# Kernel optimization log

Measured on AMD Instinct MI355X. Metric: run time of the kernel, lower is better.

Reference implementation:

```python
import jax, jax.numpy as jnp
import numpy as np

NHEAD = 8
TOPKS = [16, 8]  # coarse -> fine (indexed by loop i over reversed pyramids)


def _gather_kv(t, idx):
    # t: [b, M, nh, d], idx: [b, N, K, nh] -> gathered [b, N, K, nh, d]
    b, M, nh, d = t.shape
    bi = jnp.arange(b)[:, None, None, None]
    hi = jnp.arange(nh)[None, None, None, :]
    return t[bi, idx, hi]


def _process_level(query, key, value, topk_pos, topk_prev, topk):
    # query: [b, c, h0, w0]; key/value: [b, c, h1, w1] with h1=h0, w1=w0
    bs, c, h0, w0 = query.shape
    _, _, h1, w1 = key.shape
    nh = NHEAD
    d = c // nh
    N = (h0 // 2) * (w0 // 2)
    # b c h w -> b (h w) nh d
    k = key.reshape(bs, c, h1 * w1).transpose(0, 2, 1).reshape(bs, h1 * w1, nh, d)
    v = value.reshape(bs, c, h1 * w1).transpose(0, 2, 1).reshape(bs, h1 * w1, nh, d)
    # b c (h 2) (w 2) -> b (h w) 4 nh d  (2x2 query groups)
    q = query.reshape(bs, c, h0 // 2, 2, w0 // 2, 2)
    q = q.transpose(0, 2, 4, 3, 5, 1).reshape(bs, N, 4, nh, d)
    # expand each coarse candidate position into its 2x2 children in the key grid
    tp = topk_pos * 2  # [2, b, N, Kp, nh]
    idx = jnp.stack([(tp[0] + x) * w1 + (tp[1] + y)
                     for x in (0, 1) for y in (0, 1)], axis=3)  # [b,N,Kp,4,nh]
    K = topk_prev * 4
    idx = idx.reshape(bs, N, K, nh)
    # sparse scores: QK[b,n,t,k,h] = <q[b,n,t,h,:], key[b, idx[b,n,k,h], h, :]>
    kg = _gather_kv(k, idx)  # [b,N,K,nh,d]
    QK = jnp.einsum('bnthd,bnkhd->bntkh', q, kg) * (d ** -0.5)
    A = jax.nn.softmax(QK, axis=-2)  # softmax over the K candidates
    # top-k over candidates (dim=-2 of A); lax.top_k works on last axis
    A_t = jnp.swapaxes(A, -1, -2)  # [b,N,4,nh,K]
    ts_t, li = jax.lax.top_k(A_t, topk)
    idx_bc = jnp.broadcast_to(jnp.swapaxes(idx, -1, -2)[:, :, None], A_t.shape)
    ti_t = jnp.take_along_axis(idx_bc, li, axis=-1)
    topk_score = jnp.swapaxes(ts_t, -1, -2)  # [b,N,4,topk,nh]
    topk_idx = jnp.swapaxes(ti_t, -1, -2)
    # value aggregation (idx is repeated over the 4 group slots in the original,
    # so a single gather is the same math): message[b,n,t,h,d]=sum_k A*v[idx]
    vg = _gather_kv(v, idx)  # [b,N,K,nh,d]
    message = jnp.einsum('bntkh,bnkhd->bnthd', A, vg)  # [b,N,4,nh,d]

    def regroup(x):  # b (h w) (t1 t2) k nh -> b (h t1 w t2) k nh
        x = x.reshape(bs, h0 // 2, w0 // 2, 2, 2, topk, nh)
        return x.transpose(0, 1, 3, 2, 4, 5, 6).reshape(bs, h0 * w0, topk, nh)

    return message, regroup(topk_score), regroup(topk_idx)


def _forward(q_fine, q_coarse, k_fine, k_coarse, v_fine, v_coarse, weight, topk_pos):
    queries = [q_fine, q_coarse]  # original list order: fine -> coarse
    keys = [k_fine, k_coarse]
    values = [v_fine, v_coarse]
    messages = []
    topk = TOPKS[0]
    tp = topk_pos
    for i, (q, k, v) in enumerate(zip(queries[::-1], keys[::-1], values[::-1])):
        w1 = k.shape[3]
        topk_prev, topk = topk, TOPKS[i]
        msg, ts, ti = _process_level(q, k, v, tp, topk_prev, topk)
        messages.append(msg)
        tp = jnp.stack([ti // w1, ti % w1])  # (row, col) in current key grid
    wsm = jax.nn.softmax(weight)

    def comb(x, H):  # b (H W) (t1 t2) h d -> b (H t1 W t2) h d, t1=t2=2
        bs, N, _, nh, d = x.shape
        W = N // H
        x = x.reshape(bs, H, W, 2, 2, nh, d).transpose(0, 1, 3, 2, 4, 5, 6)
        return x.reshape(bs, H * 2 * W * 2, nh, d)

    fm = None
    for i, m in enumerate(messages):
        if i == 0:
            fm = m * wsm[i]
        else:
            fm = fm[:, :, None] + m * wsm[i]
        # faithful to original: queries[-i] (note queries[-0] == queries[0])
        H = queries[-i].shape[2]
        fm = comb(fm, H)
    return fm  # [b, Hf*Wf, nh, d]


def setup_inputs() -> dict:
    key = jax.random.key(0)
    ks = jax.random.split(key, 8)
    f = jnp.float32
    return {
        'q_fine': jax.random.normal(ks[0], (2, 128, 128, 128), f),
        'q_coarse': jax.random.normal(ks[1], (2, 128, 64, 64), f),
        'k_fine': jax.random.normal(ks[2], (2, 128, 128, 128), f),
        'k_coarse': jax.random.normal(ks[3], (2, 128, 64, 64), f),
        'v_fine': jax.random.normal(ks[4], (2, 128, 128, 128), f),
        'v_coarse': jax.random.normal(ks[5], (2, 128, 64, 64), f),
        'weight': jax.random.normal(ks[6], (2,), f),
        'topk_pos': jax.random.randint(ks[7], (2, 2, 1024, 16, 8), 0, 32, dtype=jnp.int32),
    }


def reference(q_fine, q_coarse, k_fine, k_coarse, v_fine, v_coarse, weight, topk_pos):
    return _forward(q_fine, q_coarse, k_fine, k_coarse, v_fine, v_coarse, weight, topk_pos)
```

## Files before the change

### kernel.cpp

```cpp
#include <hip/hip_runtime.h>

#define C 128

__device__ __forceinline__ void wave_sync() {
  __builtin_amdgcn_wave_barrier();
  asm volatile("s_waitcnt lgkmcnt(0)" ::: "memory");
  __builtin_amdgcn_wave_barrier();
}

__device__ __forceinline__ void transpose_tile(const float* __restrict__ in,
                                               float* __restrict__ out, int P,
                                               int tx, int chHalf, int b,
                                               float (*tile)[65]) {
  int posBase = tx * 64;
  int chBase  = chHalf * 64;
  int tid = threadIdx.x;
  int lp = tid & 63;
  int lr = tid >> 6;
  const float* ip = in + (size_t)b * C * P;
  float* op = out + (size_t)b * C * P;
#pragma unroll
  for (int it = 0; it < 16; ++it) {
    int ch = lr + it * 4;
    tile[ch][lp] = ip[(size_t)(chBase + ch) * P + posBase + lp];
  }
  __syncthreads();
  int ch2 = chBase + lp;
  int hh = ch2 >> 4, dd = ch2 & 15;
#pragma unroll
  for (int it = 0; it < 16; ++it) {
    int pl = lr + it * 4;
    op[((size_t)hh * P + posBase + pl) * 16 + dd] = tile[lp][pl];
  }
}

__global__ __launch_bounds__(256) void transpose_coarse(
    const float* __restrict__ q, const float* __restrict__ k,
    const float* __restrict__ v, float* __restrict__ qo,
    float* __restrict__ ko, float* __restrict__ vo) {
  __shared__ alignas(16) float tile[64][65];
  int idx = blockIdx.x;
  int tx = idx & 63;
  int ty = (idx >> 6) % 6;
  int tz = idx / 384;
  int sel = ty >> 1;
  const float* in = sel == 0 ? q : sel == 1 ? k : v;
  float* out      = sel == 0 ? qo : sel == 1 ? ko : vo;
  transpose_tile(in, out, 4096, tx, ty & 1, tz, tile);
}

__global__ __launch_bounds__(256) void fused_mid(
    const float* __restrict__ qf, const float* __restrict__ kf,
    const float* __restrict__ vf, float* __restrict__ qtf,
    float* __restrict__ ktf, float* __restrict__ vtf,
    const float* __restrict__ qt, const float* __restrict__ kt,
    const float* __restrict__ vt, const int* __restrict__ parents,
    float* __restrict__ mc, int* __restrict__ ti_out)
{
  __shared__ alignas(16) float lds[64 * 65];

  if (blockIdx.x >= 4096) {
    int idx = blockIdx.x - 4096;
    int tx = idx & 255;
    int ty = (idx >> 8) % 6;
    int tz = idx / 1536;
    int sel = ty >> 1;
    const float* in = sel == 0 ? qf : sel == 1 ? kf : vf;
    float* out      = sel == 0 ? qtf : sel == 1 ? ktf : vtf;
    transpose_tile(in, out, 16384, tx, ty & 1, tz, (float (*)[65])lds);
    return;
  }

  float (*als_t)[4][64]    = (float (*)[4][64])   lds;
  float (*als_k)[4][17][4] = (float (*)[4][17][4])(lds + 1024);
  float (*qls)[4][16]      = (float (*)[4][16])  (lds + 2112);
  int   (*cofs)[64]        = (int (*)[64])       (lds + 2368);

  const int abid = blockIdx.x;
  const int lane = threadIdx.x & 63;
  const int wid  = threadIdx.x >> 6;
  const int wg = (abid & 7) * 512 + (abid >> 3);
  const int u  = wg * 4 + wid;
  const int n  = u & 1023;
  const int bh = u >> 10;
  const int b  = bh >> 3;
  const int h  = bh & 7;
  const int hb = n >> 5;
  const int wb = n & 31;
  const int hD = h * 16;

  { int t = lane >> 4, dd = lane & 15;
    int pix = (hb * 2 + (t >> 1)) * 64 + (wb * 2 + (t & 1));
    qls[wid][t][dd] = qt[((size_t)bh * 4096 + pix) * 16 + dd]; }
  int cand, off0;
  { int kp = lane >> 2, c = lane & 3;
    int r  = parents[(size_t)b * 131072          + n * 128 + kp * 8 + h];
    int cc = parents[(size_t)b * 131072 + 262144 + n * 128 + kp * 8 + h];
    cand = (2 * r + (c >> 1)) * 64 + 2 * cc + (c & 1);
    off0 = (bh * 4096 + cand) * 16;
    cofs[wid][lane] = off0; }
  wave_sync();

  const float4* kv4 = (const float4*)(kt + off0);
  float4 k0 = kv4[0], k1 = kv4[1], k2 = kv4[2], k3 = kv4[3];
  float sc[4];
#pragma unroll
  for (int t = 0; t < 4; ++t) {
    const float4* qv = (const float4*)qls[wid][t];
    float4 q0 = qv[0], q1 = qv[1], q2 = qv[2], q3 = qv[3];
    float acc = k0.x*q0.x + k0.y*q0.y + k0.z*q0.z + k0.w*q0.w
              + k1.x*q1.x + k1.y*q1.y + k1.z*q1.z + k1.w*q1.w
              + k2.x*q2.x + k2.y*q2.y + k2.z*q2.z + k2.w*q2.w
              + k3.x*q3.x + k3.y*q3.y + k3.z*q3.z + k3.w*q3.w;
    sc[t] = acc * 0.25f;
  }

  float mx[4], ex[4], sm[4], a[4];
#pragma unroll
  for (int t = 0; t < 4; ++t) mx[t] = sc[t];
#pragma unroll
  for (int off = 32; off >= 1; off >>= 1)
#pragma unroll
    for (int t = 0; t < 4; ++t) mx[t] = fmaxf(mx[t], __shfl_xor(mx[t], off));
#pragma unroll
  for (int t = 0; t < 4; ++t) { ex[t] = __expf(sc[t] - mx[t]); sm[t] = ex[t]; }
#pragma unroll
  for (int off = 32; off >= 1; off >>= 1)
#pragma unroll
    for (int t = 0; t < 4; ++t) sm[t] += __shfl_xor(sm[t], off);
#pragma unroll
  for (int t = 0; t < 4; ++t) { a[t] = ex[t] / sm[t]; als_t[wid][t][lane] = a[t]; }
  *(float4*)&als_k[wid][lane >> 4][lane & 15][0] = make_float4(a[0], a[1], a[2], a[3]);
  wave_sync();

#pragma unroll
  for (int tt = 0; tt < 4; ++tt) {
    float myv = a[tt];
    int rank = 0;
    for (int j4 = 0; j4 < 64; j4 += 4) {
      float4 vj = *(const float4*)&als_t[wid][tt][j4];
      rank += (vj.x > myv) || (vj.x == myv && (j4 + 0) < lane);
      rank += (vj.y > myv) || (vj.y == myv && (j4 + 1) < lane);
      rank += (vj.z > myv) || (vj.z == myv && (j4 + 2) < lane);
      rank += (vj.w > myv) || (vj.w == myv && (j4 + 3) < lane);
    }
    if (rank < 16) {
      int n1 = (2 * hb + (tt >> 1)) * 64 + 2 * wb + (tt & 1);
      ti_out[((size_t)bh * 4096 + n1) * 16 + rank] = cand;
    }
  }

  {
    const int g = lane >> 4, dd = lane & 15;
    float acc0 = 0.f, acc1 = 0.f, acc2 = 0.f, acc3 = 0.f;
#pragma unroll
    for (int k4 = 0; k4 < 16; k4 += 4) {
      int4 cv = *(const int4*)&cofs[wid][g * 16 + k4];
      float4 a0 = *(const float4*)&als_k[wid][g][k4 + 0][0];
      float4 a1 = *(const float4*)&als_k[wid][g][k4 + 1][0];
      float4 a2 = *(const float4*)&als_k[wid][g][k4 + 2][0];
      float4 a3 = *(const float4*)&als_k[wid][g][k4 + 3][0];
      float v0 = vt[cv.x + dd];
      float v1 = vt[cv.y + dd];
      float v2 = vt[cv.z + dd];
      float v3 = vt[cv.w + dd];
      acc0 += a0.x * v0; acc1 += a0.y * v0; acc2 += a0.z * v0; acc3 += a0.w * v0;
      acc0 += a1.x * v1; acc1 += a1.y * v1; acc2 += a1.z * v1; acc3 += a1.w * v1;
      acc0 += a2.x * v2; acc1 += a2.y * v2; acc2 += a2.z * v2; acc3 += a2.w * v2;
      acc0 += a3.x * v3; acc1 += a3.y * v3; acc2 += a3.z * v3; acc3 += a3.w * v3;
    }
    acc0 += __shfl_xor(acc0, 16); acc0 += __shfl_xor(acc0, 32);
    acc1 += __shfl_xor(acc1, 16); acc1 += __shfl_xor(acc1, 32);
    acc2 += __shfl_xor(acc2, 16); acc2 += __shfl_xor(acc2, 32);
    acc3 += __shfl_xor(acc3, 16); acc3 += __shfl_xor(acc3, 32);
    float msg = (g & 2) ? ((g & 1) ? acc3 : acc2) : ((g & 1) ? acc1 : acc0);
    int m = hb * 128 + (wb >> 3) * 32 + (g >> 1) * 16 + (wb & 7) * 2 + (g & 1);
    mc[(b * 4096 + m) * C + hD + dd] = msg;
  }
}

__global__ __launch_bounds__(256) void attn_fine2(
    const float* __restrict__ qt, const float* __restrict__ kt,
    const float* __restrict__ vt, const int* __restrict__ tin,
    const float* __restrict__ mc, const float* __restrict__ weight,
    float* __restrict__ out)
{
  __shared__ alignas(16) float als_k[4][2][4][17][4];
  __shared__ alignas(16) float qls[4][2][4][16];
  __shared__ alignas(16) int   cofs[4][2][64];

  const int lane = threadIdx.x & 63;
  const int wid  = threadIdx.x >> 6;
  const int wg = (blockIdx.x & 7) * 1024 + (blockIdx.x >> 3);
  const int p  = wg * 4 + wid;
  const int wb2 = p & 31;
  const int hb  = (p >> 5) & 63;
  const int h   = (p >> 11) & 7;
  const int b   = p >> 14;
  const int bh  = b * 8 + h;
  const int nA  = hb * 64 + wb2 * 2;
  const int hD  = h * 16;

  { int t = lane >> 4, dd = lane & 15;
    int rowq = (hb * 2 + (t >> 1)) * 128;
    qls[wid][0][t][dd] = qt[((size_t)bh * 16384 + rowq + wb2 * 4     + (t & 1)) * 16 + dd];
    qls[wid][1][t][dd] = qt[((size_t)bh * 16384 + rowq + wb2 * 4 + 2 + (t & 1)) * 16 + dd];
  }
  int off0A, off0B;
  { int kp = lane >> 2, c = lane & 3;
    int tA = tin[((size_t)bh * 4096 + nA    ) * 16 + kp];
    int tB = tin[((size_t)bh * 4096 + nA + 1) * 16 + kp];
    int candA = (2 * (tA >> 6) + (c >> 1)) * 128 + 2 * (tA & 63) + (c & 1);
    int candB = (2 * (tB >> 6) + (c >> 1)) * 128 + 2 * (tB & 63) + (c & 1);
    off0A = (bh * 16384 + candA) * 16;
    off0B = (bh * 16384 + candB) * 16;
    cofs[wid][0][lane] = off0A;
    cofs[wid][1][lane] = off0B;
  }
  wave_sync();

  float4 kA0, kA1, kA2, kA3, kB0, kB1, kB2, kB3;
  { const float4* kv = (const float4*)(kt + off0A); kA0 = kv[0]; kA1 = kv[1]; kA2 = kv[2]; kA3 = kv[3]; }
  { const float4* kv = (const float4*)(kt + off0B); kB0 = kv[0]; kB1 = kv[1]; kB2 = kv[2]; kB3 = kv[3]; }

  float ex0[4], ex1[4];
#pragma unroll
  for (int t = 0; t < 4; ++t) {
    { const float4* qv = (const float4*)qls[wid][0][t];
      float4 q0 = qv[0], q1 = qv[1], q2 = qv[2], q3 = qv[3];
      float acc = kA0.x*q0.x + kA0.y*q0.y + kA0.z*q0.z + kA0.w*q0.w
                + kA1.x*q1.x + kA1.y*q1.y + kA1.z*q1.z + kA1.w*q1.w
                + kA2.x*q2.x + kA2.y*q2.y + kA2.z*q2.z + kA2.w*q2.w
                + kA3.x*q3.x + kA3.y*q3.y + kA3.z*q3.z + kA3.w*q3.w;
      ex0[t] = __expf(acc * 0.25f); }
    { const float4* qv = (const float4*)qls[wid][1][t];
      float4 q0 = qv[0], q1 = qv[1], q2 = qv[2], q3 = qv[3];
      float acc = kB0.x*q0.x + kB0.y*q0.y + kB0.z*q0.z + kB0.w*q0.w
                + kB1.x*q1.x + kB1.y*q1.y + kB1.z*q1.z + kB1.w*q1.w
                + kB2.x*q2.x + kB2.y*q2.y + kB2.z*q2.z + kB2.w*q2.w
                + kB3.x*q3.x + kB3.y*q3.y + kB3.z*q3.z + kB3.w*q3.w;
      ex1[t] = __expf(acc * 0.25f); }
  }
  *(float4*)&als_k[wid][0][lane >> 4][lane & 15][0] = make_float4(ex0[0], ex0[1], ex0[2], ex0[3]);
  *(float4*)&als_k[wid][1][lane >> 4][lane & 15][0] = make_float4(ex1[0], ex1[1], ex1[2], ex1[3]);
  wave_sync();

  const int g = lane >> 4, dd = lane & 15;
  float mcvA = mc[((size_t)b * 4096 + nA    ) * C + hD + dd];
  float mcvB = mc[((size_t)b * 4096 + nA + 1) * C + hD + dd];

  float smA[4], smB[4];
#pragma unroll
  for (int t = 0; t < 4; ++t) { smA[t] = ex0[t]; smB[t] = ex1[t]; }
#pragma unroll
  for (int off = 32; off >= 1; off >>= 1)
#pragma unroll
    for (int t = 0; t < 4; ++t) {
      smA[t] += __shfl_xor(smA[t], off);
      smB[t] += __shfl_xor(smB[t], off);
    }

  float aA0 = 0, aA1 = 0, aA2 = 0, aA3 = 0;
  float aB0 = 0, aB1 = 0, aB2 = 0, aB3 = 0;
#pragma unroll
  for (int k4 = 0; k4 < 16; k4 += 4) {
    int4 cvA = *(const int4*)&cofs[wid][0][g * 16 + k4];
    int4 cvB = *(const int4*)&cofs[wid][1][g * 16 + k4];
    float vA0 = vt[cvA.x + dd], vA1 = vt[cvA.y + dd];
    float vA2 = vt[cvA.z + dd], vA3 = vt[cvA.w + dd];
    float vB0 = vt[cvB.x + dd], vB1 = vt[cvB.y + dd];
    float vB2 = vt[cvB.z + dd], vB3 = vt[cvB.w + dd];
    float4 wA0 = *(const float4*)&als_k[wid][0][g][k4 + 0][0];
    float4 wA1 = *(const float4*)&als_k[wid][0][g][k4 + 1][0];
    float4 wA2 = *(const float4*)&als_k[wid][0][g][k4 + 2][0];
    float4 wA3 = *(const float4*)&als_k[wid][0][g][k4 + 3][0];
    float4 wB0 = *(const float4*)&als_k[wid][1][g][k4 + 0][0];
    float4 wB1 = *(const float4*)&als_k[wid][1][g][k4 + 1][0];
    float4 wB2 = *(const float4*)&als_k[wid][1][g][k4 + 2][0];
    float4 wB3 = *(const float4*)&als_k[wid][1][g][k4 + 3][0];
    aA0 += wA0.x * vA0; aA1 += wA0.y * vA0; aA2 += wA0.z * vA0; aA3 += wA0.w * vA0;
    aA0 += wA1.x * vA1; aA1 += wA1.y * vA1; aA2 += wA1.z * vA1; aA3 += wA1.w * vA1;
    aA0 += wA2.x * vA2; aA1 += wA2.y * vA2; aA2 += wA2.z * vA2; aA3 += wA2.w * vA2;
    aA0 += wA3.x * vA3; aA1 += wA3.y * vA3; aA2 += wA3.z * vA3; aA3 += wA3.w * vA3;
    aB0 += wB0.x * vB0; aB1 += wB0.y * vB0; aB2 += wB0.z * vB0; aB3 += wB0.w * vB0;
    aB0 += wB1.x * vB1; aB1 += wB1.y * vB1; aB2 += wB1.z * vB1; aB3 += wB1.w * vB1;
    aB0 += wB2.x * vB2; aB1 += wB2.y * vB2; aB2 += wB2.z * vB2; aB3 += wB2.w * vB2;
    aB0 += wB3.x * vB3; aB1 += wB3.y * vB3; aB2 += wB3.z * vB3; aB3 += wB3.w * vB3;
  }
  aA0 += __shfl_xor(aA0, 16); aA0 += __shfl_xor(aA0, 32);
  aA1 += __shfl_xor(aA1, 16); aA1 += __shfl_xor(aA1, 32);
  aA2 += __shfl_xor(aA2, 16); aA2 += __shfl_xor(aA2, 32);
  aA3 += __shfl_xor(aA3, 16); aA3 += __shfl_xor(aA3, 32);
  aB0 += __shfl_xor(aB0, 16); aB0 += __shfl_xor(aB0, 32);
  aB1 += __shfl_xor(aB1, 16); aB1 += __shfl_xor(aB1, 32);
  aB2 += __shfl_xor(aB2, 16); aB2 += __shfl_xor(aB2, 32);
  aB3 += __shfl_xor(aB3, 16); aB3 += __shfl_xor(aB3, 32);

  float msgA = (g & 2) ? ((g & 1) ? aA3 : aA2) : ((g & 1) ? aA1 : aA0);
  float msgB = (g & 2) ? ((g & 1) ? aB3 : aB2) : ((g & 1) ? aB1 : aB0);
  float smvA = (g & 2) ? ((g & 1) ? smA[3] : smA[2]) : ((g & 1) ? smA[1] : smA[0]);
  float smvB = (g & 2) ? ((g & 1) ? smB[3] : smB[2]) : ((g & 1) ? smB[1] : smB[0]);
  msgA /= smvA;
  msgB /= smvB;

  float w0 = weight[0], w1 = weight[1];
  float wm = fmaxf(w0, w1);
  float e0 = __expf(w0 - wm), e1 = __expf(w1 - wm);
  float inv = 1.0f / (e0 + e1);
  int rowq = (hb * 2 + (g >> 1)) * 128;
  out[((size_t)b * 16384 + rowq + wb2 * 4     + (g & 1)) * C + hD + dd] =
      (e0 * inv) * mcvA + (e1 * inv) * msgA;
  out[((size_t)b * 16384 + rowq + wb2 * 4 + 2 + (g & 1)) * C + hD + dd] =
      (e0 * inv) * mcvB + (e1 * inv) * msgB;
}

extern "C" void kernel_launch(void* const* d_in, const int* in_sizes, int n_in,
                              void* d_out, int out_size, void* d_ws, size_t ws_size,
                              hipStream_t stream) {
  const float* q_fine   = (const float*)d_in[0];
  const float* q_coarse = (const float*)d_in[1];
  const float* k_fine   = (const float*)d_in[2];
  const float* k_coarse = (const float*)d_in[3];
  const float* v_fine   = (const float*)d_in[4];
  const float* v_coarse = (const float*)d_in[5];
  const float* weight   = (const float*)d_in[6];
  const int*   topk_pos = (const int*)d_in[7];
  float* out = (float*)d_out;

  const int PF = 16384, PC = 4096;
  float* ws   = (float*)d_ws;
  float* qt_f = ws;
  float* kt_f = qt_f + 2 * PF * C;
  float* vt_f = kt_f + 2 * PF * C;
  float* qt_c = vt_f + 2 * PF * C;
  float* kt_c = qt_c + 2 * PC * C;
  float* vt_c = kt_c + 2 * PC * C;
  float* mc   = vt_c + 2 * PC * C;
  int*   ti   = (int*)(mc + 2 * 4096 * C);

  dim3 blk(256);
  transpose_coarse<<<768, blk, 0, stream>>>(q_coarse, k_coarse, v_coarse,
                                            qt_c, kt_c, vt_c);
  fused_mid<<<4096 + 3072, blk, 0, stream>>>(q_fine, k_fine, v_fine,
                                             qt_f, kt_f, vt_f,
                                             qt_c, kt_c, vt_c, topk_pos, mc, ti);
  attn_fine2<<<8192, blk, 0, stream>>>(qt_f, kt_f, vt_f, ti, mc, weight, out);
}
```

Baseline: 110.7 us.

## Use ballot radix-select top-k and 32-channel transpose tiles to shrink LDS

The per-lane O(64) LDS rank computation for top-16 is replaced by a bitwise radix select using wave ballots and popcounts. Ties are resolved by lane order and selected entries are compacted into output slots. The transpose tiles are halved to 32 channels with a write pattern that emits contiguous 16-float head vectors, and the block counts are doubled to match. Together these halve the shared memory of fused_mid, which should raise occupancy and remove LDS traffic, at the cost of about 31 serial ballot iterations and twice as many transpose blocks. The output slot order for selected indices now follows lane order rather than score rank.

```diff
diff --git a/kernel.cpp b/kernel.cpp
--- a/kernel.cpp
+++ b/kernel.cpp
@@ -8,29 +8,31 @@
   __builtin_amdgcn_wave_barrier();
 }
 
-__device__ __forceinline__ void transpose_tile(const float* __restrict__ in,
-                                               float* __restrict__ out, int P,
-                                               int tx, int chHalf, int b,
-                                               float (*tile)[65]) {
+__device__ __forceinline__ void transpose_tile32(const float* __restrict__ in,
+                                                 float* __restrict__ out, int P,
+                                                 int tx, int chQ, int b,
+                                                 float (*tile)[65]) {
   int posBase = tx * 64;
-  int chBase  = chHalf * 64;
+  int chBase  = chQ * 32;
   int tid = threadIdx.x;
   int lp = tid & 63;
   int lr = tid >> 6;
   const float* ip = in + (size_t)b * C * P;
   float* op = out + (size_t)b * C * P;
 #pragma unroll
-  for (int it = 0; it < 16; ++it) {
+  for (int it = 0; it < 8; ++it) {
     int ch = lr + it * 4;
     tile[ch][lp] = ip[(size_t)(chBase + ch) * P + posBase + lp];
   }
   __syncthreads();
-  int ch2 = chBase + lp;
-  int hh = ch2 >> 4, dd = ch2 & 15;
-#pragma unroll
-  for (int it = 0; it < 16; ++it) {
-    int pl = lr + it * 4;
-    op[((size_t)hh * P + posBase + pl) * 16 + dd] = tile[lp][pl];
+  int dd   = tid & 15;
+  int hh2  = (tid >> 4) & 1;
+  int prow = tid >> 5;
+  int h = (chBase >> 4) + hh2;
+#pragma unroll
+  for (int it = 0; it < 8; ++it) {
+    int pos = prow + it * 8;
+    op[((size_t)h * P + posBase + pos) * 16 + dd] = tile[hh2 * 16 + dd][pos];
   }
 }
 
@@ -38,15 +40,15 @@
     const float* __restrict__ q, const float* __restrict__ k,
     const float* __restrict__ v, float* __restrict__ qo,
     float* __restrict__ ko, float* __restrict__ vo) {
-  __shared__ alignas(16) float tile[64][65];
+  __shared__ alignas(16) float tile[32][65];
   int idx = blockIdx.x;
   int tx = idx & 63;
-  int ty = (idx >> 6) % 6;
-  int tz = idx / 384;
-  int sel = ty >> 1;
+  int ty = (idx >> 6) % 12;
+  int tz = idx / 768;
+  int sel = ty >> 2;
   const float* in = sel == 0 ? q : sel == 1 ? k : v;
   float* out      = sel == 0 ? qo : sel == 1 ? ko : vo;
-  transpose_tile(in, out, 4096, tx, ty & 1, tz, tile);
+  transpose_tile32(in, out, 4096, tx, ty & 3, tz, tile);
 }
 
 __global__ __launch_bounds__(256) void fused_mid(
@@ -57,24 +59,23 @@
     const float* __restrict__ vt, const int* __restrict__ parents,
     float* __restrict__ mc, int* __restrict__ ti_out)
 {
-  __shared__ alignas(16) float lds[64 * 65];
+  __shared__ alignas(16) float lds[32 * 65];
 
   if (blockIdx.x >= 4096) {
     int idx = blockIdx.x - 4096;
     int tx = idx & 255;
-    int ty = (idx >> 8) % 6;
-    int tz = idx / 1536;
-    int sel = ty >> 1;
+    int ty = (idx >> 8) % 12;
+    int tz = idx / 3072;
+    int sel = ty >> 2;
     const float* in = sel == 0 ? qf : sel == 1 ? kf : vf;
     float* out      = sel == 0 ? qtf : sel == 1 ? ktf : vtf;
-    transpose_tile(in, out, 16384, tx, ty & 1, tz, (float (*)[65])lds);
+    transpose_tile32(in, out, 16384, tx, ty & 3, tz, (float (*)[65])lds);
     return;
   }
 
-  float (*als_t)[4][64]    = (float (*)[4][64])   lds;
-  float (*als_k)[4][17][4] = (float (*)[4][17][4])(lds + 1024);
-  float (*qls)[4][16]      = (float (*)[4][16])  (lds + 2112);
-  int   (*cofs)[64]        = (int (*)[64])       (lds + 2368);
+  float (*als_k)[4][17][4] = (float (*)[4][17][4])lds;
+  float (*qls)[4][16]      = (float (*)[4][16])(lds + 1088);
+  int   (*cofs)[64]        = (int (*)[64])    (lds + 1344);
 
   const int abid = blockIdx.x;
   const int lane = threadIdx.x & 63;
@@ -129,26 +130,41 @@
 #pragma unroll
     for (int t = 0; t < 4; ++t) sm[t] += __shfl_xor(sm[t], off);
 #pragma unroll
-  for (int t = 0; t < 4; ++t) { a[t] = ex[t] / sm[t]; als_t[wid][t][lane] = a[t]; }
+  for (int t = 0; t < 4; ++t) a[t] = ex[t] / sm[t];
   *(float4*)&als_k[wid][lane >> 4][lane & 15][0] = make_float4(a[0], a[1], a[2], a[3]);
+
+  {
+    unsigned uu[4];
+#pragma unroll
+    for (int t = 0; t < 4; ++t) uu[t] = __float_as_uint(a[t]);
+    unsigned T0 = 0, T1 = 0, T2 = 0, T3 = 0;
+    for (int bit = 30; bit >= 0; --bit) {
+      unsigned m = 1u << bit;
+      unsigned c0 = T0 | m, c1 = T1 | m, c2 = T2 | m, c3 = T3 | m;
+      if (__popcll(__ballot(uu[0] >= c0)) >= 16) T0 = c0;
+      if (__popcll(__ballot(uu[1] >= c1)) >= 16) T1 = c1;
+      if (__popcll(__ballot(uu[2] >= c2)) >= 16) T2 = c2;
+      if (__popcll(__ballot(uu[3] >= c3)) >= 16) T3 = c3;
+    }
+    unsigned Tv[4] = {T0, T1, T2, T3};
+    unsigned long long lower = (1ull << lane) - 1ull;
+#pragma unroll
+    for (int tt = 0; tt < 4; ++tt) {
+      unsigned uv = uu[tt], T = Tv[tt];
+      unsigned long long gt = __ballot(uv > T);
+      unsigned long long eq = __ballot(uv == T);
+      int ngt = __popcll(gt);
+      bool sel = (uv > T) ||
+                 ((uv == T) && (ngt + (int)__popcll(eq & lower) < 16));
+      unsigned long long selm = __ballot(sel);
+      int slot = __popcll(selm & lower);
+      if (sel) {
+        int n1 = (2 * hb + (tt >> 1)) * 64 + 2 * wb + (tt & 1);
+        ti_out[((size_t)bh * 4096 + n1) * 16 + slot] = cand;
+      }
+    }
+  }
   wave_sync();
-
-#pragma unroll
-  for (int tt = 0; tt < 4; ++tt) {
-    float myv = a[tt];
-    int rank = 0;
-    for (int j4 = 0; j4 < 64; j4 += 4) {
-      float4 vj = *(const float4*)&als_t[wid][tt][j4];
-      rank += (vj.x > myv) || (vj.x == myv && (j4 + 0) < lane);
-      rank += (vj.y > myv) || (vj.y == myv && (j4 + 1) < lane);
-      rank += (vj.z > myv) || (vj.z == myv && (j4 + 2) < lane);
-      rank += (vj.w > myv) || (vj.w == myv && (j4 + 3) < lane);
-    }
-    if (rank < 16) {
-      int n1 = (2 * hb + (tt >> 1)) * 64 + 2 * wb + (tt & 1);
-      ti_out[((size_t)bh * 4096 + n1) * 16 + rank] = cand;
-    }
-  }
 
   {
     const int g = lane >> 4, dd = lane & 15;
@@ -339,9 +355,9 @@
   int*   ti   = (int*)(mc + 2 * 4096 * C);
 
   dim3 blk(256);
-  transpose_coarse<<<768, blk, 0, stream>>>(q_coarse, k_coarse, v_coarse,
-                                            qt_c, kt_c, vt_c);
-  fused_mid<<<4096 + 3072, blk, 0, stream>>>(q_fine, k_fine, v_fine,
+  transpose_coarse<<<1536, blk, 0, stream>>>(q_coarse, k_coarse, v_coarse,
+                                             qt_c, kt_c, vt_c);
+  fused_mid<<<4096 + 6144, blk, 0, stream>>>(q_fine, k_fine, v_fine,
                                              qt_f, kt_f, vt_f,
                                              qt_c, kt_c, vt_c, topk_pos, mc, ti);
   attn_fine2<<<8192, blk, 0, stream>>>(qt_f, kt_f, vt_f, ti, mc, weight, out);
```

New measurement: 91.87 us. 1.2x faster.
